# Performance work log

Measured on AMD Instinct MI355X. Metric: run time of the kernel, lower is better.

## Reference

```python
import jax, jax.numpy as jnp
import numpy as np

H = 2048      # hidden_size
NH = 32       # num_heads
NKV = 8       # num_kv_heads
HD = H // NH  # head_dim = 64
G = NH // NKV # num_kv_groups = 4
T = 2048      # seq_len
S = int(T * 0.5)  # num_compressed = 1024
DEPTH = 2
I = 5632      # GatedMLP intermediate size
B = 1
EPS = 1e-6


def _rms_norm(x, w):
    return x * jax.lax.rsqrt(jnp.mean(x * x, axis=-1, keepdims=True) + EPS) * w


def setup_inputs() -> dict:
    key = jax.random.key(0)
    ks = jax.random.split(key, 8)
    s = 0.02
    return {
        "hidden_states": jax.random.normal(ks[0], (B, T, H), jnp.float32),
        "q_w": jax.random.normal(ks[1], (H, H), jnp.float32) * s,
        "k_w": jax.random.normal(ks[2], (NKV * HD, H), jnp.float32) * s,
        "v_w": jax.random.normal(ks[3], (NKV * HD, H), jnp.float32) * s,
        "o_w": jax.random.normal(ks[4], (H, H), jnp.float32) * s,
        "attn_norm_w": jnp.ones((H,), jnp.float32),
        "mlp_norm_w": jnp.ones((H,), jnp.float32),
        "gate_w": jax.random.normal(ks[5], (I, H), jnp.float32) * s,
        "up_w": jax.random.normal(ks[6], (I, H), jnp.float32) * s,
        "down_w": jax.random.normal(ks[7], (H, I), jnp.float32) * s,
    }


def reference(hidden_states, q_w, k_w, v_w, o_w, attn_norm_w, mlp_norm_w,
              gate_w, up_w, down_w):
    b, t, h = hidden_states.shape
    scale = HD ** -0.5
    # suffix init: compressed tokens are the last S tokens
    ct = hidden_states[:, -S:, :]  # [B, S, H]
    for _ in range(DEPTH):
        residual = jnp.concatenate([hidden_states, ct], axis=1)  # [B, T+S, H]
        x = _rms_norm(ct, attn_norm_w)
        q = (x @ q_w.T).reshape(b, S, NH, HD)              # [B,S,NH,HD]
        k = (residual @ k_w.T).reshape(b, t + S, NKV, HD)  # [B,T+S,NKV,HD]
        v = (residual @ v_w.T).reshape(b, t + S, NKV, HD)
        # GQA: repeat_interleave over head dim
        k = jnp.repeat(k, G, axis=2)  # [B,T+S,NH,HD]
        v = jnp.repeat(v, G, axis=2)
        scores = jnp.einsum('bsnk,btnk->bsnt', q, k) * scale  # [B,S,NH,T+S]
        attn = jax.nn.softmax(scores, axis=-1)
        o = jnp.einsum('bsnt,btnk->bsnk', attn, v).reshape(b, S, h)
        ct = o @ o_w.T + ct
        y = _rms_norm(ct, mlp_norm_w)
        mlp = (jax.nn.silu(y @ gate_w.T) * (y @ up_w.T)) @ down_w.T
        ct = mlp + y  # note: residual adds to the *normed* tokens, as in source
    return ct
```

## Files before the change

### kernel.cpp

```cpp
#include <hip/hip_runtime.h>

typedef __attribute__((ext_vector_type(8))) short short8;
typedef __attribute__((ext_vector_type(4))) float f32x4;
typedef __attribute__((ext_vector_type(4))) unsigned short us4;
typedef __attribute__((ext_vector_type(8))) unsigned short us8;

__device__ __forceinline__ unsigned short f2bf(float f) {
  union { float f; unsigned u; } v; v.f = f;
  unsigned r = v.u + 0x7fffu + ((v.u >> 16) & 1u);
  return (unsigned short)(r >> 16);
}
__device__ __forceinline__ float bf2f(unsigned short b) {
  union { unsigned u; float f; } v; v.u = ((unsigned)b) << 16;
  return v.f;
}
__device__ __forceinline__ float fexp2(float x) {
  float r; asm("v_exp_f32 %0, %1" : "=v"(r) : "v"(x)); return r;
}
__device__ __forceinline__ us8 cvt8v(f32x4 a, f32x4 b) {
  us8 o;
  o[0] = f2bf(a[0]); o[1] = f2bf(a[1]); o[2] = f2bf(a[2]); o[3] = f2bf(a[3]);
  o[4] = f2bf(b[0]); o[5] = f2bf(b[1]); o[6] = f2bf(b[2]); o[7] = f2bf(b[3]);
  return o;
}

__device__ __forceinline__ void gload_lds16(const void* g, void* l) {
  __builtin_amdgcn_global_load_lds((const __attribute__((address_space(1))) void*)g,
                                   (__attribute__((address_space(3))) void*)l,
                                   16, 0, 0);
}

#define VMW6() asm volatile("s_waitcnt vmcnt(6)" ::: "memory")
#define VMW0() asm volatile("s_waitcnt vmcnt(0)" ::: "memory")
#define LGKM0() asm volatile("s_waitcnt lgkmcnt(0)" ::: "memory")

template<int R>
__device__ __forceinline__ void stage64(const unsigned short* g, int K, int k0,
                                        unsigned short* lds, int tid) {
  const int lane = tid & 63, w = tid >> 6;
  constexpr int RW = R / 4;
  constexpr int NL = RW / 8;
#pragma unroll
  for (int i = 0; i < NL; i++) {
    const int r0 = w * RW + i * 8;
    const int row = r0 + (lane >> 3);
    const int colb = (((lane & 7) ^ (lane >> 3)) << 4);
    gload_lds16((const char*)(g + (size_t)row * K + k0) + colb, lds + r0 * 64);
  }
}
__device__ __forceinline__ short8 lds_frag(const unsigned short* t, int row, int cb) {
  return *(const short8*)((const char*)t + row * 128 + (cb ^ ((row & 7) << 4)));
}

__global__ __launch_bounds__(256) void gemm_split(
    const unsigned short* __restrict__ A,
    const unsigned short* __restrict__ B,
    int K,
    float* __restrict__ P,
    int ldo)
{
  constexpr int BM = 64, BN = 128, BK = 64;
  __shared__ __align__(16) unsigned short sA[3][BM * BK];
  __shared__ __align__(16) unsigned short sB[3][BN * BK];
  const int tid = threadIdx.x;
  const int lane = tid & 63, w = tid >> 6;
  const int wr = w >> 1, wc = w & 1;
  const int ln = lane & 15, qo = lane >> 4;
  const size_t m0 = (size_t)blockIdx.y * BM, n0 = (size_t)blockIdx.x * BN;
  const int koff = blockIdx.z * (K >> 1);
  const unsigned short* Ab = A + m0 * K;
  const unsigned short* Bb = B + n0 * K;

  const f32x4 z4 = {0.f, 0.f, 0.f, 0.f};
  f32x4 acc[2][4];
#pragma unroll
  for (int i = 0; i < 2; i++)
#pragma unroll
    for (int j = 0; j < 4; j++) acc[i][j] = z4;

  const int nt = K / (2 * BK);
  stage64<BM>(Ab, K, koff, sA[0], tid);
  stage64<BN>(Bb, K, koff, sB[0], tid);
  stage64<BM>(Ab, K, koff + BK, sA[1], tid);
  stage64<BN>(Bb, K, koff + BK, sB[1], tid);

  int cur = 0;
  for (int t = 0; t < nt; ++t) {
    if (t == nt - 1) VMW0(); else VMW6();
    __builtin_amdgcn_s_barrier();
    asm volatile("" ::: "memory");
    if (t + 2 < nt) {
      const int nx = (cur == 0) ? 2 : cur - 1;
      stage64<BM>(Ab, K, koff + (t + 2) * BK, sA[nx], tid);
      stage64<BN>(Bb, K, koff + (t + 2) * BK, sB[nx], tid);
    }
    const unsigned short* cA = sA[cur];
    const unsigned short* cB = sB[cur];
#pragma unroll
    for (int ks = 0; ks < 2; ks++) {
      short8 af[2], bfv[4];
#pragma unroll
      for (int mi = 0; mi < 2; mi++)
        af[mi] = lds_frag(cA, wr * 32 + mi * 16 + ln, ks * 64 + qo * 16);
#pragma unroll
      for (int ni = 0; ni < 4; ni++)
        bfv[ni] = lds_frag(cB, wc * 64 + ni * 16 + ln, ks * 64 + qo * 16);
      __builtin_amdgcn_s_setprio(1);
#pragma unroll
      for (int mi = 0; mi < 2; mi++)
#pragma unroll
        for (int ni = 0; ni < 4; ni++)
          acc[mi][ni] = __builtin_amdgcn_mfma_f32_16x16x32_bf16(af[mi], bfv[ni], acc[mi][ni], 0, 0, 0);
      __builtin_amdgcn_s_setprio(0);
    }
    cur = (cur == 2) ? 0 : cur + 1;
  }

  float* Pz = P + (size_t)blockIdx.z * 1024 * (size_t)ldo;
#pragma unroll
  for (int mi = 0; mi < 2; mi++) {
#pragma unroll
    for (int ni = 0; ni < 4; ni++) {
      const size_t row4 = m0 + wr * 32 + mi * 16 + qo * 4;
      const size_t col  = n0 + wc * 64 + ni * 16 + ln;
#pragma unroll
      for (int r = 0; r < 4; r++)
        Pz[(row4 + r) * (size_t)ldo + col] = acc[mi][ni][r];
    }
  }
}

__global__ __launch_bounds__(256) void gemm_gu(
    const unsigned short* __restrict__ A,
    const unsigned short* __restrict__ B,
    unsigned short* __restrict__ outb)
{
  __shared__ __align__(16) unsigned short sA[2][128 * 64];
  __shared__ __align__(16) unsigned short sB[2][128 * 64];
  const int tid = threadIdx.x;
  const int lane = tid & 63, w = tid >> 6;
  const int wr = w >> 1, wc = w & 1;
  const int ln = lane & 15, qo = lane >> 4;
  const int bid = blockIdx.x;
  const int swz = (bid & 7) * 88 + (bid >> 3);
  const size_t m0 = (size_t)(swz & 7) * 128;
  const size_t n0 = (size_t)(swz >> 3) * 128;
  const unsigned short* Ab = A + m0 * 2048;
  const unsigned short* Bb = B + n0 * 2048;

  const f32x4 z4 = {0.f, 0.f, 0.f, 0.f};
  f32x4 acc[4][4];
#pragma unroll
  for (int i = 0; i < 4; i++)
#pragma unroll
    for (int j = 0; j < 4; j++) acc[i][j] = z4;

  stage64<128>(Ab, 2048, 0, sA[0], tid);
  stage64<128>(Bb, 2048, 0, sB[0], tid);

  for (int t = 0; t < 32; ++t) {
    const int cur = t & 1;
    VMW0();
    __builtin_amdgcn_s_barrier();
    asm volatile("" ::: "memory");
    if (t + 1 < 32) {
      stage64<128>(Ab, 2048, (t + 1) * 64, sA[cur ^ 1], tid);
      stage64<128>(Bb, 2048, (t + 1) * 64, sB[cur ^ 1], tid);
    }
    const unsigned short* cA = sA[cur];
    const unsigned short* cB = sB[cur];
#pragma unroll
    for (int ks = 0; ks < 2; ks++) {
      short8 af[4], bfv[4];
#pragma unroll
      for (int mi = 0; mi < 4; mi++)
        af[mi] = lds_frag(cA, wr * 64 + mi * 16 + ln, ks * 64 + qo * 16);
#pragma unroll
      for (int ni = 0; ni < 4; ni++)
        bfv[ni] = lds_frag(cB, wc * 64 + ni * 16 + ln, ks * 64 + qo * 16);
      __builtin_amdgcn_s_setprio(1);
#pragma unroll
      for (int mi = 0; mi < 4; mi++)
#pragma unroll
        for (int ni = 0; ni < 4; ni++)
          acc[mi][ni] = __builtin_amdgcn_mfma_f32_16x16x32_bf16(af[mi], bfv[ni], acc[mi][ni], 0, 0, 0);
      __builtin_amdgcn_s_setprio(0);
    }
  }

#pragma unroll
  for (int mi = 0; mi < 4; mi++) {
#pragma unroll
    for (int j = 0; j < 2; j++) {
      const size_t row4 = m0 + wr * 64 + mi * 16 + qo * 4;
      const size_t cg = (n0 >> 1) + wc * 32 + j * 16 + ln;
#pragma unroll
      for (int r = 0; r < 4; r++) {
        float g = acc[mi][2 * j][r], u = acc[mi][2 * j + 1][r];
        outb[(row4 + r) * 5632 + cg] = f2bf(g / (1.f + __expf(-g)) * u);
      }
    }
  }
}

template<int SPLIT>
__global__ __launch_bounds__(256) void gemm_dual(
    const unsigned short* __restrict__ A,
    const unsigned short* __restrict__ B0,
    const unsigned short* __restrict__ B1,
    int K,
    unsigned short* __restrict__ out0,
    unsigned short* __restrict__ out1,
    float* __restrict__ P,
    int ld0, int ld1)
{
  constexpr int BM = 64, BN = 64, BK = 64;
  __shared__ __align__(16) unsigned short sA[3][BM * BK];
  __shared__ __align__(16) unsigned short sB0[3][BN * BK];
  __shared__ __align__(16) unsigned short sB1[3][BN * BK];
  const int tid = threadIdx.x;
  const int lane = tid & 63, w = tid >> 6;
  const int wr = w >> 1, wc = w & 1;
  const int ln = lane & 15, qo = lane >> 4;
  const size_t m0 = (size_t)blockIdx.y * BM, n0 = (size_t)blockIdx.x * BN;
  const int koff = SPLIT ? blockIdx.z * (K >> 1) : 0;
  const unsigned short* Ab = A + m0 * K;
  const unsigned short* B0b = B0 + n0 * K;
  const unsigned short* B1b = B1 + n0 * K;

  const f32x4 z4 = {0.f, 0.f, 0.f, 0.f};
  f32x4 acc0[2][2], acc1[2][2];
#pragma unroll
  for (int i = 0; i < 2; i++)
#pragma unroll
    for (int j = 0; j < 2; j++) { acc0[i][j] = z4; acc1[i][j] = z4; }

  const int nt = SPLIT ? K / (2 * BK) : K / BK;
  stage64<BM>(Ab, K, koff, sA[0], tid);
  stage64<BN>(B0b, K, koff, sB0[0], tid);
  stage64<BN>(B1b, K, koff, sB1[0], tid);
  stage64<BM>(Ab, K, koff + BK, sA[1], tid);
  stage64<BN>(B0b, K, koff + BK, sB0[1], tid);
  stage64<BN>(B1b, K, koff + BK, sB1[1], tid);

  int cur = 0;
  for (int t = 0; t < nt; ++t) {
    if (t == nt - 1) VMW0(); else VMW6();
    __builtin_amdgcn_s_barrier();
    asm volatile("" ::: "memory");
    if (t + 2 < nt) {
      const int nx = (cur == 0) ? 2 : cur - 1;
      stage64<BM>(Ab, K, koff + (t + 2) * BK, sA[nx], tid);
      stage64<BN>(B0b, K, koff + (t + 2) * BK, sB0[nx], tid);
      stage64<BN>(B1b, K, koff + (t + 2) * BK, sB1[nx], tid);
    }
    const unsigned short* cA = sA[cur];
    const unsigned short* cB0 = sB0[cur];
    const unsigned short* cB1 = sB1[cur];
#pragma unroll
    for (int ks = 0; ks < 2; ks++) {
      short8 af[2], b0f[2], b1f[2];
#pragma unroll
      for (int mi = 0; mi < 2; mi++)
        af[mi] = lds_frag(cA, wr * 32 + mi * 16 + ln, ks * 64 + qo * 16);
#pragma unroll
      for (int ni = 0; ni < 2; ni++) {
        b0f[ni] = lds_frag(cB0, wc * 32 + ni * 16 + ln, ks * 64 + qo * 16);
        b1f[ni] = lds_frag(cB1, wc * 32 + ni * 16 + ln, ks * 64 + qo * 16);
      }
      __builtin_amdgcn_s_setprio(1);
#pragma unroll
      for (int mi = 0; mi < 2; mi++)
#pragma unroll
        for (int ni = 0; ni < 2; ni++) {
          acc0[mi][ni] = __builtin_amdgcn_mfma_f32_16x16x32_bf16(af[mi], b0f[ni], acc0[mi][ni], 0, 0, 0);
          acc1[mi][ni] = __builtin_amdgcn_mfma_f32_16x16x32_bf16(af[mi], b1f[ni], acc1[mi][ni], 0, 0, 0);
        }
      __builtin_amdgcn_s_setprio(0);
    }
    cur = (cur == 2) ? 0 : cur + 1;
  }

#pragma unroll
  for (int mi = 0; mi < 2; mi++) {
#pragma unroll
    for (int ni = 0; ni < 2; ni++) {
      const size_t row4 = m0 + wr * 32 + mi * 16 + qo * 4;
      const size_t col  = n0 + wc * 32 + ni * 16 + ln;
      if (SPLIT) {
        float* Pz = P + (size_t)blockIdx.z * 1048576;
#pragma unroll
        for (int r = 0; r < 4; r++) {
          Pz[(row4 + r) * 1024 + col] = acc0[mi][ni][r];
          Pz[(row4 + r) * 1024 + 512 + col] = acc1[mi][ni][r];
        }
      } else {
#pragma unroll
        for (int r = 0; r < 4; r++)
          out0[(row4 + r) * (size_t)ld0 + col] = f2bf(acc0[mi][ni][r]);
        us4 pk;
        pk[0] = f2bf(acc1[mi][ni][0]); pk[1] = f2bf(acc1[mi][ni][1]);
        pk[2] = f2bf(acc1[mi][ni][2]); pk[3] = f2bf(acc1[mi][ni][3]);
        *(us4*)&out1[col * (size_t)ld1 + row4] = pk;
      }
    }
  }
}

__global__ __launch_bounds__(256) void combine_kv(
    const float* __restrict__ P,
    unsigned short* __restrict__ kB,
    unsigned short* __restrict__ vt)
{
  const int j = blockIdx.x * 256 + threadIdx.x;
  {
    const int row = j >> 9, col = j & 511;
    float v = P[row * 1024 + col] + P[1048576 + row * 1024 + col];
    kB[row * 512 + col] = f2bf(v);
  }
  {
    const int hd = j >> 10, key = j & 1023;
    float v0 = P[key * 1024 + 512 + hd] + P[1048576 + key * 1024 + 512 + hd];
    vt[(size_t)hd * 3072 + key] = f2bf(v0);
  }
}

__global__ __launch_bounds__(256) void attn_k(
    const float* __restrict__ Pq,
    const unsigned short* __restrict__ Kb,
    const unsigned short* __restrict__ Vt,
    unsigned short* __restrict__ Op,
    float* __restrict__ Ml)
{
  __shared__ __align__(16) unsigned short sK[2][64 * 64];
  __shared__ __align__(16) unsigned short sV[2][64 * 64];
  __shared__ __align__(16) unsigned short sP[64 * 64];
  const int tid = threadIdx.x;
  const int lane = tid & 63, w = tid >> 6;
  const int ln = lane & 15, qo = lane >> 4;
  const int head = blockIdx.y, kvh = head >> 2;
  const int half = blockIdx.z;
  const int qw = blockIdx.x * 64 + w * 16;
  const int key0 = half * 1536;

  const float QS = 0.18033688011112042f;
  const float* qr = Pq + (size_t)(qw + ln) * 2048 + head * 64;
  short8 qf[2];
#pragma unroll
  for (int kc = 0; kc < 2; kc++) {
    const float* q0 = qr + kc * 32 + qo * 8;
    f32x4 a0 = *(const f32x4*)(q0);
    f32x4 a1 = *(const f32x4*)(q0 + 4);
    f32x4 b0 = *(const f32x4*)(q0 + 2097152);
    f32x4 b1 = *(const f32x4*)(q0 + 2097152 + 4);
    short8 t;
    t[0] = (short)f2bf((a0[0] + b0[0]) * QS); t[1] = (short)f2bf((a0[1] + b0[1]) * QS);
    t[2] = (short)f2bf((a0[2] + b0[2]) * QS); t[3] = (short)f2bf((a0[3] + b0[3]) * QS);
    t[4] = (short)f2bf((a1[0] + b1[0]) * QS); t[5] = (short)f2bf((a1[1] + b1[1]) * QS);
    t[6] = (short)f2bf((a1[2] + b1[2]) * QS); t[7] = (short)f2bf((a1[3] + b1[3]) * QS);
    qf[kc] = t;
  }

  const f32x4 z4 = {0.f, 0.f, 0.f, 0.f};
  f32x4 oacc[4] = {z4, z4, z4, z4};
  float mrun = -1e30f, lrun = 0.f;

  const unsigned short* Kg = Kb + kvh * 64;
  const unsigned short* Vg = Vt + (size_t)(kvh * 64) * 3072;

  stage64<64>(Kg + (size_t)key0 * 512, 512, 0, sK[0], tid);
  stage64<64>(Vg, 3072, key0, sV[0], tid);

  for (int t = 0; t < 24; ++t) {
    const int cur = t & 1;
    VMW0();
    __builtin_amdgcn_s_barrier();
    asm volatile("" ::: "memory");
    if (t + 1 < 24) {
      stage64<64>(Kg + (size_t)(key0 + (t + 1) * 64) * 512, 512, 0, sK[cur ^ 1], tid);
      stage64<64>(Vg, 3072, key0 + (t + 1) * 64, sV[cur ^ 1], tid);
    }

    f32x4 sacc[4] = {z4, z4, z4, z4};
#pragma unroll
    for (int kc = 0; kc < 2; kc++) {
      short8 kf[4];
#pragma unroll
      for (int mi = 0; mi < 4; mi++)
        kf[mi] = lds_frag(sK[cur], mi * 16 + ln, kc * 64 + qo * 16);
      __builtin_amdgcn_s_setprio(1);
#pragma unroll
      for (int mi = 0; mi < 4; mi++)
        sacc[mi] = __builtin_amdgcn_mfma_f32_16x16x32_bf16(kf[mi], qf[kc], sacc[mi], 0, 0, 0);
      __builtin_amdgcn_s_setprio(0);
    }

    float tm = -1e30f;
#pragma unroll
    for (int mi = 0; mi < 4; mi++) {
      float a0 = fmaxf(sacc[mi][0], sacc[mi][1]);
      float a1 = fmaxf(sacc[mi][2], sacc[mi][3]);
      tm = fmaxf(tm, fmaxf(a0, a1));
    }
    tm = fmaxf(tm, __shfl_xor(tm, 16));
    tm = fmaxf(tm, __shfl_xor(tm, 32));

    if (!__all(tm <= mrun + 11.f)) {
      const float mn = fmaxf(mrun, tm);
      const float al = fexp2(mrun - mn);
      lrun *= al;
      mrun = mn;
#pragma unroll
      for (int r = 0; r < 4; r++) {
        float ar = __shfl(al, qo * 4 + r);
#pragma unroll
        for (int ni = 0; ni < 4; ni++) oacc[ni][r] *= ar;
      }
    }

    float ts = 0.f;
#pragma unroll
    for (int mi = 0; mi < 4; mi++) {
      us4 pk;
#pragma unroll
      for (int r = 0; r < 4; r++) {
        float pv = fexp2(sacc[mi][r] - mrun);
        ts += pv;
        pk[r] = f2bf(pv);
      }
      const int row = w * 16 + ln;
      const int g16 = (2 * mi + (qo >> 1)) ^ (ln & 7);
      *(us4*)((char*)sP + row * 128 + (g16 << 4) + ((qo & 1) << 3)) = pk;
    }
    ts += __shfl_xor(ts, 16);
    ts += __shfl_xor(ts, 32);
    lrun += ts;

#pragma unroll
    for (int ks = 0; ks < 2; ks++) {
      short8 pf = lds_frag(sP, w * 16 + ln, ks * 64 + qo * 16);
      short8 vf[4];
#pragma unroll
      for (int ni = 0; ni < 4; ni++)
        vf[ni] = lds_frag(sV[cur], ni * 16 + ln, ks * 64 + qo * 16);
      __builtin_amdgcn_s_setprio(1);
#pragma unroll
      for (int ni = 0; ni < 4; ni++)
        oacc[ni] = __builtin_amdgcn_mfma_f32_16x16x32_bf16(pf, vf[ni], oacc[ni], 0, 0, 0);
      __builtin_amdgcn_s_setprio(0);
    }
    LGKM0();
  }

  if (qo == 0)
    *(float2*)&Ml[((size_t)(half * 32 + head) * 1024 + qw + ln) * 2] =
        make_float2(mrun, lrun);
#pragma unroll
  for (int r = 0; r < 4; r++)
#pragma unroll
    for (int ni = 0; ni < 4; ni++)
      Op[(size_t)half * 2097152 + (size_t)(qw + qo * 4 + r) * 2048 + head * 64 + ni * 16 + ln] =
          f2bf(oacc[ni][r]);
}

__global__ __launch_bounds__(256) void attn_combine(
    const unsigned short* __restrict__ Op,
    const float* __restrict__ Ml,
    unsigned short* __restrict__ O)
{
  const int f = blockIdx.x * 256 + threadIdx.x;
  const int q = f >> 9;
  const int c = (f & 511) * 4;
  const int head = c >> 6;
  const float2 ml0 = *(const float2*)&Ml[((size_t)head * 1024 + q) * 2];
  const float2 ml1 = *(const float2*)&Ml[((size_t)(32 + head) * 1024 + q) * 2];
  const float m = fmaxf(ml0.x, ml1.x);
  const float w0 = fexp2(ml0.x - m), w1 = fexp2(ml1.x - m);
  const float inv = 1.f / (w0 * ml0.y + w1 * ml1.y);
  const us4 o0 = *(const us4*)&Op[(size_t)q * 2048 + c];
  const us4 o1 = *(const us4*)&Op[2097152 + (size_t)q * 2048 + c];
  us4 o;
#pragma unroll
  for (int j = 0; j < 4; j++)
    o[j] = f2bf((w0 * bf2f(o0[j]) + w1 * bf2f(o1[j])) * inv);
  *(us4*)&O[(size_t)q * 2048 + c] = o;
}

__global__ __launch_bounds__(256) void rmsnorm_k(const float* __restrict__ in,
                                                 const float* __restrict__ w,
                                                 unsigned short* __restrict__ out) {
  const int row = blockIdx.x;
  const int tid = threadIdx.x;
  const float* x = in + (size_t)row * 2048;
  float4 a = ((const float4*)x)[tid * 2];
  float4 b = ((const float4*)x)[tid * 2 + 1];
  float ss = a.x * a.x + a.y * a.y + a.z * a.z + a.w * a.w +
             b.x * b.x + b.y * b.y + b.z * b.z + b.w * b.w;
#pragma unroll
  for (int d = 1; d < 64; d <<= 1) ss += __shfl_xor(ss, d);
  __shared__ float red[4];
  if ((tid & 63) == 0) red[tid >> 6] = ss;
  __syncthreads();
  float sc = rsqrtf((red[0] + red[1] + red[2] + red[3]) * (1.f / 2048.f) + 1e-6f);
  float4 wa = ((const float4*)w)[tid * 2];
  float4 wb = ((const float4*)w)[tid * 2 + 1];
  us4 o1, o2;
  o1[0] = f2bf(a.x * sc * wa.x); o1[1] = f2bf(a.y * sc * wa.y);
  o1[2] = f2bf(a.z * sc * wa.z); o1[3] = f2bf(a.w * sc * wa.w);
  o2[0] = f2bf(b.x * sc * wb.x); o2[1] = f2bf(b.y * sc * wb.y);
  o2[2] = f2bf(b.z * sc * wb.z); o2[3] = f2bf(b.w * sc * wb.w);
  us4* op = (us4*)&out[(size_t)row * 2048 + tid * 8];
  op[0] = o1; op[1] = o2;
}

__global__ __launch_bounds__(256) void rmsnorm_add_k(
    float* __restrict__ ctf, const float* __restrict__ P,
    const float* __restrict__ w, unsigned short* __restrict__ out) {
  const int row = blockIdx.x;
  const int tid = threadIdx.x;
  const size_t base = (size_t)row * 2048 + tid * 8;
  float t[8];
  float4 c0 = *(const float4*)&ctf[base], c1 = *(const float4*)&ctf[base + 4];
  float4 p0 = *(const float4*)&P[base], p1 = *(const float4*)&P[base + 4];
  float4 q0 = *(const float4*)&P[base + 2097152], q1 = *(const float4*)&P[base + 2097152 + 4];
  t[0] = c0.x + p0.x + q0.x; t[1] = c0.y + p0.y + q0.y;
  t[2] = c0.z + p0.z + q0.z; t[3] = c0.w + p0.w + q0.w;
  t[4] = c1.x + p1.x + q1.x; t[5] = c1.y + p1.y + q1.y;
  t[6] = c1.z + p1.z + q1.z; t[7] = c1.w + p1.w + q1.w;
  *(float4*)&ctf[base] = make_float4(t[0], t[1], t[2], t[3]);
  *(float4*)&ctf[base + 4] = make_float4(t[4], t[5], t[6], t[7]);
  float ss = 0.f;
#pragma unroll
  for (int i = 0; i < 8; i++) ss += t[i] * t[i];
#pragma unroll
  for (int d = 1; d < 64; d <<= 1) ss += __shfl_xor(ss, d);
  __shared__ float red[4];
  if ((tid & 63) == 0) red[tid >> 6] = ss;
  __syncthreads();
  float sc = rsqrtf((red[0] + red[1] + red[2] + red[3]) * (1.f / 2048.f) + 1e-6f);
  us4 o1, o2;
#pragma unroll
  for (int i = 0; i < 4; i++) o1[i] = f2bf(t[i] * sc * w[tid * 8 + i]);
#pragma unroll
  for (int i = 0; i < 4; i++) o2[i] = f2bf(t[4 + i] * sc * w[tid * 8 + 4 + i]);
  us4* op = (us4*)&out[base];
  op[0] = o1; op[1] = o2;
}

__global__ __launch_bounds__(256) void rmsnorm_add2_k(
    const float* __restrict__ P, unsigned short* __restrict__ yb,
    float* __restrict__ ctf, unsigned short* __restrict__ ctb,
    const float* __restrict__ w) {
  const int row = blockIdx.x;
  const int tid = threadIdx.x;
  const size_t base = (size_t)row * 2048 + tid * 8;
  float t[8];
  float4 p0 = *(const float4*)&P[base], p1 = *(const float4*)&P[base + 4];
  float4 q0 = *(const float4*)&P[base + 2097152], q1 = *(const float4*)&P[base + 2097152 + 4];
  us4 y0 = *(const us4*)&yb[base], y1 = *(const us4*)&yb[base + 4];
  t[0] = p0.x + q0.x + bf2f(y0[0]); t[1] = p0.y + q0.y + bf2f(y0[1]);
  t[2] = p0.z + q0.z + bf2f(y0[2]); t[3] = p0.w + q0.w + bf2f(y0[3]);
  t[4] = p1.x + q1.x + bf2f(y1[0]); t[5] = p1.y + q1.y + bf2f(y1[1]);
  t[6] = p1.z + q1.z + bf2f(y1[2]); t[7] = p1.w + q1.w + bf2f(y1[3]);
  *(float4*)&ctf[base] = make_float4(t[0], t[1], t[2], t[3]);
  *(float4*)&ctf[base + 4] = make_float4(t[4], t[5], t[6], t[7]);
  us4 cb0, cb1;
#pragma unroll
  for (int i = 0; i < 4; i++) { cb0[i] = f2bf(t[i]); cb1[i] = f2bf(t[4 + i]); }
  *(us4*)&ctb[base] = cb0; *(us4*)&ctb[base + 4] = cb1;
  float ss = 0.f;
#pragma unroll
  for (int i = 0; i < 8; i++) ss += t[i] * t[i];
#pragma unroll
  for (int d = 1; d < 64; d <<= 1) ss += __shfl_xor(ss, d);
  __shared__ float red[4];
  if ((tid & 63) == 0) red[tid >> 6] = ss;
  __syncthreads();
  float sc = rsqrtf((red[0] + red[1] + red[2] + red[3]) * (1.f / 2048.f) + 1e-6f);
  us4 o1, o2;
#pragma unroll
  for (int i = 0; i < 4; i++) o1[i] = f2bf(t[i] * sc * w[tid * 8 + i]);
#pragma unroll
  for (int i = 0; i < 4; i++) o2[i] = f2bf(t[4 + i] * sc * w[tid * 8 + 4 + i]);
  us4* op = (us4*)&yb[base];
  op[0] = o1; op[1] = o2;
}

__global__ __launch_bounds__(256) void combine2_k(
    const float* __restrict__ P, const unsigned short* __restrict__ yb,
    float* __restrict__ out) {
  const int j = blockIdx.x * 256 + threadIdx.x;
  float4 p0 = ((const float4*)P)[j];
  float4 p1 = ((const float4*)P)[j + 524288];
  us4 y = ((const us4*)yb)[j];
  float4 o;
  o.x = p0.x + p1.x + bf2f(y[0]); o.y = p0.y + p1.y + bf2f(y[1]);
  o.z = p0.z + p1.z + bf2f(y[2]); o.w = p0.w + p1.w + bf2f(y[3]);
  ((float4*)out)[j] = o;
}

__global__ __launch_bounds__(256) void cvt_all(
    const float* __restrict__ hid, const float* __restrict__ qw,
    const float* __restrict__ kw, const float* __restrict__ vw,
    const float* __restrict__ ow, const float* __restrict__ gw,
    const float* __restrict__ uw, const float* __restrict__ dw,
    unsigned short* __restrict__ hb, unsigned short* __restrict__ qwB,
    unsigned short* __restrict__ kwB, unsigned short* __restrict__ vwB,
    unsigned short* __restrict__ owB, unsigned short* __restrict__ guB,
    unsigned short* __restrict__ dwB,
    float* __restrict__ ctf, unsigned short* __restrict__ ctb)
{
  const int gid = blockIdx.x * 256 + threadIdx.x;
  const int gs = gridDim.x * 256;
  for (int i = gid; i < 524288; i += gs) {
    f32x4 a = __builtin_nontemporal_load(&((const f32x4*)hid)[2 * i]);
    f32x4 b = __builtin_nontemporal_load(&((const f32x4*)hid)[2 * i + 1]);
    us8 o = cvt8v(a, b);
    ((us8*)hb)[i] = o;
    if (i >= 262144) {
      ((f32x4*)ctf)[2 * (i - 262144)] = a;
      ((f32x4*)ctf)[2 * (i - 262144) + 1] = b;
      ((us8*)ctb)[i - 262144] = o;
    }
  }
  for (int i = gid; i < 524288; i += gs) {
    f32x4 a = __builtin_nontemporal_load(&((const f32x4*)qw)[2 * i]);
    f32x4 b = __builtin_nontemporal_load(&((const f32x4*)qw)[2 * i + 1]);
    ((us8*)qwB)[i] = cvt8v(a, b);
  }
  for (int i = gid; i < 131072; i += gs) {
    f32x4 a = __builtin_nontemporal_load(&((const f32x4*)kw)[2 * i]);
    f32x4 b = __builtin_nontemporal_load(&((const f32x4*)kw)[2 * i + 1]);
    ((us8*)kwB)[i] = cvt8v(a, b);
  }
  for (int i = gid; i < 131072; i += gs) {
    f32x4 a = __builtin_nontemporal_load(&((const f32x4*)vw)[2 * i]);
    f32x4 b = __builtin_nontemporal_load(&((const f32x4*)vw)[2 * i + 1]);
    ((us8*)vwB)[i] = cvt8v(a, b);
  }
  for (int i = gid; i < 524288; i += gs) {
    f32x4 a = __builtin_nontemporal_load(&((const f32x4*)ow)[2 * i]);
    f32x4 b = __builtin_nontemporal_load(&((const f32x4*)ow)[2 * i + 1]);
    ((us8*)owB)[i] = cvt8v(a, b);
  }
  for (int i = gid; i < 1441792; i += gs) {
    f32x4 a = __builtin_nontemporal_load(&((const f32x4*)gw)[2 * i]);
    f32x4 b = __builtin_nontemporal_load(&((const f32x4*)gw)[2 * i + 1]);
    const int row = i >> 8, c8 = i & 255;
    const int drow = ((row >> 4) << 5) + (row & 15);
    ((us8*)guB)[(drow << 8) + c8] = cvt8v(a, b);
  }
  for (int i = gid; i < 1441792; i += gs) {
    f32x4 a = __builtin_nontemporal_load(&((const f32x4*)uw)[2 * i]);
    f32x4 b = __builtin_nontemporal_load(&((const f32x4*)uw)[2 * i + 1]);
    const int row = i >> 8, c8 = i & 255;
    const int drow = ((row >> 4) << 5) + (row & 15) + 16;
    ((us8*)guB)[(drow << 8) + c8] = cvt8v(a, b);
  }
  for (int i = gid; i < 1441792; i += gs) {
    f32x4 a = __builtin_nontemporal_load(&((const f32x4*)dw)[2 * i]);
    f32x4 b = __builtin_nontemporal_load(&((const f32x4*)dw)[2 * i + 1]);
    ((us8*)dwB)[i] = cvt8v(a, b);
  }
}

extern "C" void kernel_launch(void* const* d_in, const int* in_sizes, int n_in,
                              void* d_out, int out_size, void* d_ws, size_t ws_size,
                              hipStream_t stream) {
  (void)in_sizes; (void)n_in; (void)out_size; (void)ws_size;
  const float* hidden = (const float*)d_in[0];
  const float* q_w  = (const float*)d_in[1];
  const float* k_w  = (const float*)d_in[2];
  const float* v_w  = (const float*)d_in[3];
  const float* o_w  = (const float*)d_in[4];
  const float* a_nw = (const float*)d_in[5];
  const float* m_nw = (const float*)d_in[6];
  const float* g_w  = (const float*)d_in[7];
  const float* u_w  = (const float*)d_in[8];
  const float* dn_w = (const float*)d_in[9];
  float* out = (float*)d_out;

  char* p = (char*)d_ws;
  size_t off = 0;
  auto take = [&](size_t bytes) -> char* {
    char* r = p + off;
    off += (bytes + 255) & ~(size_t)255;
    return r;
  };
  float* ctf          = (float*)take((size_t)1024 * 2048 * 4);
  unsigned short* ctb = (unsigned short*)take((size_t)1024 * 2048 * 2);
  unsigned short* xb  = (unsigned short*)take((size_t)1024 * 2048 * 2);
  unsigned short* hb  = (unsigned short*)take((size_t)2048 * 2048 * 2);
  unsigned short* qwB = (unsigned short*)take((size_t)2048 * 2048 * 2);
  unsigned short* kwB = (unsigned short*)take((size_t)512 * 2048 * 2);
  unsigned short* vwB = (unsigned short*)take((size_t)512 * 2048 * 2);
  unsigned short* owB = (unsigned short*)take((size_t)2048 * 2048 * 2);
  unsigned short* guB = (unsigned short*)take((size_t)11264 * 2048 * 2);
  unsigned short* dwB = (unsigned short*)take((size_t)2048 * 5632 * 2);
  unsigned short* kB  = (unsigned short*)take((size_t)3072 * 512 * 2);
  unsigned short* vtB = (unsigned short*)take((size_t)512 * 3072 * 2);
  unsigned short* oB  = (unsigned short*)take((size_t)1024 * 2048 * 2);
  unsigned short* gtB = (unsigned short*)take((size_t)1024 * 5632 * 2);
  float* Pd           = (float*)take((size_t)2 * 1024 * 2048 * 4);

  unsigned short* Op = xb;
  float* Ml = (float*)((char*)xb + (size_t)2 * 1024 * 2048 * 2);
  float* PKV = (float*)hb;

  dim3 blk(256);
  cvt_all<<<dim3(4096), blk, 0, stream>>>(hidden, q_w, k_w, v_w, o_w, g_w, u_w, dn_w,
                                          hb, qwB, kwB, vwB, owB, guB, dwB, ctf, ctb);

  gemm_dual<0><<<dim3(8, 32), blk, 0, stream>>>(hb, kwB, vwB, 2048, kB, vtB, nullptr, 512, 3072);

  for (int it = 0; it < 2; it++) {
    if (it == 0)
      rmsnorm_k<<<dim3(1024), blk, 0, stream>>>(ctf, a_nw, xb);
    else
      rmsnorm_add2_k<<<dim3(1024), blk, 0, stream>>>(Pd, xb, ctf, ctb, a_nw);
    gemm_split<<<dim3(16, 16, 2), blk, 0, stream>>>(xb, qwB, 2048, Pd, 2048);
    gemm_dual<1><<<dim3(8, 16, 2), blk, 0, stream>>>(ctb, kwB, vwB, 2048,
                                                     nullptr, nullptr, PKV, 0, 0);
    combine_kv<<<dim3(2048), blk, 0, stream>>>(PKV, kB + (size_t)2048 * 512, vtB + 2048);
    attn_k<<<dim3(16, 32, 2), blk, 0, stream>>>(Pd, kB, vtB, Op, Ml);
    attn_combine<<<dim3(2048), blk, 0, stream>>>(Op, Ml, oB);
    gemm_split<<<dim3(16, 16, 2), blk, 0, stream>>>(oB, owB, 2048, Pd, 2048);
    rmsnorm_add_k<<<dim3(1024), blk, 0, stream>>>(ctf, Pd, m_nw, xb);
    gemm_gu<<<dim3(704), blk, 0, stream>>>(xb, guB, gtB);
    gemm_split<<<dim3(16, 16, 2), blk, 0, stream>>>(gtB, dwB, 5632, Pd, 2048);
  }
  combine2_k<<<dim3(2048), blk, 0, stream>>>(Pd, xb, out);
}
```

Baseline: 577.1 us.

## Triple-buffer gate/up GEMM and attention K/V staging with prefetch depth two

The gate/up GEMM moves from double-buffered BK=64 tiles to triple-buffered BK=32 tiles, using a new packed LDS layout that puts two 32-wide rows in one 128-byte line with an XOR swizzle. Prefetch now runs two iterations ahead and waits with a partial vmcnt instead of draining to zero. The attention kernel's K/V staging is likewise changed to three buffers with a two-ahead prefetch and partial waits. The aim is to hide global-load latency behind MFMA work, at the cost of more barriers per unit of compute in the GEMM and more LDS use in attention, which may reduce occupancy.

```diff
diff --git a/kernel.cpp b/kernel.cpp
--- a/kernel.cpp
+++ b/kernel.cpp
@@ -31,6 +31,7 @@
 }
 
 #define VMW6() asm volatile("s_waitcnt vmcnt(6)" ::: "memory")
+#define VMW4() asm volatile("s_waitcnt vmcnt(4)" ::: "memory")
 #define VMW0() asm volatile("s_waitcnt vmcnt(0)" ::: "memory")
 #define LGKM0() asm volatile("s_waitcnt lgkmcnt(0)" ::: "memory")
 
@@ -50,6 +51,29 @@
 }
 __device__ __forceinline__ short8 lds_frag(const unsigned short* t, int row, int cb) {
   return *(const short8*)((const char*)t + row * 128 + (cb ^ ((row & 7) << 4)));
+}
+
+template<int GR>
+__device__ __forceinline__ void stage32p(const unsigned short* g, int K, int k0,
+                                         unsigned short* lds, int tid) {
+  const int lane = tid & 63, w = tid >> 6;
+  constexpr int LR = GR / 2;
+  constexpr int RW = LR / 4;
+  constexpr int NL = RW / 8;
+#pragma unroll
+  for (int i = 0; i < NL; i++) {
+    const int R0 = w * RW + i * 8;
+    const int R = R0 + (lane >> 3);
+    const int gg = (lane & 7) ^ (R & 7);
+    const int grow = 2 * R + (gg >> 2);
+    const int gcol = (gg & 3) * 8;
+    gload_lds16(g + (size_t)grow * K + k0 + gcol, lds + R0 * 64);
+  }
+}
+__device__ __forceinline__ short8 frag32p(const unsigned short* t, int grow, int qo) {
+  const int R = grow >> 1;
+  const int g16 = (((grow & 1) << 2) + qo) ^ (R & 7);
+  return *(const short8*)((const char*)t + R * 128 + (g16 << 4));
 }
 
 __global__ __launch_bounds__(256) void gemm_split(
@@ -135,8 +159,8 @@
     const unsigned short* __restrict__ B,
     unsigned short* __restrict__ outb)
 {
-  __shared__ __align__(16) unsigned short sA[2][128 * 64];
-  __shared__ __align__(16) unsigned short sB[2][128 * 64];
+  __shared__ __align__(16) unsigned short sA[3][64 * 64];
+  __shared__ __align__(16) unsigned short sB[3][64 * 64];
   const int tid = threadIdx.x;
   const int lane = tid & 63, w = tid >> 6;
   const int wr = w >> 1, wc = w & 1;
@@ -155,37 +179,39 @@
 #pragma unroll
     for (int j = 0; j < 4; j++) acc[i][j] = z4;
 
-  stage64<128>(Ab, 2048, 0, sA[0], tid);
-  stage64<128>(Bb, 2048, 0, sB[0], tid);
-
-  for (int t = 0; t < 32; ++t) {
-    const int cur = t & 1;
-    VMW0();
+  const int nt = 64;
+  stage32p<128>(Ab, 2048, 0, sA[0], tid);
+  stage32p<128>(Bb, 2048, 0, sB[0], tid);
+  stage32p<128>(Ab, 2048, 32, sA[1], tid);
+  stage32p<128>(Bb, 2048, 32, sB[1], tid);
+
+  int cur = 0;
+  for (int t = 0; t < nt; ++t) {
+    if (t == nt - 1) VMW0(); else VMW4();
     __builtin_amdgcn_s_barrier();
     asm volatile("" ::: "memory");
-    if (t + 1 < 32) {
-      stage64<128>(Ab, 2048, (t + 1) * 64, sA[cur ^ 1], tid);
-      stage64<128>(Bb, 2048, (t + 1) * 64, sB[cur ^ 1], tid);
+    if (t + 2 < nt) {
+      const int nx = (cur == 0) ? 2 : cur - 1;
+      stage32p<128>(Ab, 2048, (t + 2) * 32, sA[nx], tid);
+      stage32p<128>(Bb, 2048, (t + 2) * 32, sB[nx], tid);
     }
     const unsigned short* cA = sA[cur];
     const unsigned short* cB = sB[cur];
-#pragma unroll
-    for (int ks = 0; ks < 2; ks++) {
-      short8 af[4], bfv[4];
-#pragma unroll
-      for (int mi = 0; mi < 4; mi++)
-        af[mi] = lds_frag(cA, wr * 64 + mi * 16 + ln, ks * 64 + qo * 16);
+    short8 af[4], bfv[4];
+#pragma unroll
+    for (int mi = 0; mi < 4; mi++)
+      af[mi] = frag32p(cA, wr * 64 + mi * 16 + ln, qo);
+#pragma unroll
+    for (int ni = 0; ni < 4; ni++)
+      bfv[ni] = frag32p(cB, wc * 64 + ni * 16 + ln, qo);
+    __builtin_amdgcn_s_setprio(1);
+#pragma unroll
+    for (int mi = 0; mi < 4; mi++)
 #pragma unroll
       for (int ni = 0; ni < 4; ni++)
-        bfv[ni] = lds_frag(cB, wc * 64 + ni * 16 + ln, ks * 64 + qo * 16);
-      __builtin_amdgcn_s_setprio(1);
-#pragma unroll
-      for (int mi = 0; mi < 4; mi++)
-#pragma unroll
-        for (int ni = 0; ni < 4; ni++)
-          acc[mi][ni] = __builtin_amdgcn_mfma_f32_16x16x32_bf16(af[mi], bfv[ni], acc[mi][ni], 0, 0, 0);
-      __builtin_amdgcn_s_setprio(0);
-    }
+        acc[mi][ni] = __builtin_amdgcn_mfma_f32_16x16x32_bf16(af[mi], bfv[ni], acc[mi][ni], 0, 0, 0);
+    __builtin_amdgcn_s_setprio(0);
+    cur = (cur == 2) ? 0 : cur + 1;
   }
 
 #pragma unroll
@@ -332,8 +358,8 @@
     unsigned short* __restrict__ Op,
     float* __restrict__ Ml)
 {
-  __shared__ __align__(16) unsigned short sK[2][64 * 64];
-  __shared__ __align__(16) unsigned short sV[2][64 * 64];
+  __shared__ __align__(16) unsigned short sK[3][64 * 64];
+  __shared__ __align__(16) unsigned short sV[3][64 * 64];
   __shared__ __align__(16) unsigned short sP[64 * 64];
   const int tid = threadIdx.x;
   const int lane = tid & 63, w = tid >> 6;
@@ -370,15 +396,18 @@
 
   stage64<64>(Kg + (size_t)key0 * 512, 512, 0, sK[0], tid);
   stage64<64>(Vg, 3072, key0, sV[0], tid);
-
+  stage64<64>(Kg + (size_t)(key0 + 64) * 512, 512, 0, sK[1], tid);
+  stage64<64>(Vg, 3072, key0 + 64, sV[1], tid);
+
+  int cur = 0;
   for (int t = 0; t < 24; ++t) {
-    const int cur = t & 1;
-    VMW0();
+    if (t == 23) VMW0(); else VMW4();
     __builtin_amdgcn_s_barrier();
     asm volatile("" ::: "memory");
-    if (t + 1 < 24) {
-      stage64<64>(Kg + (size_t)(key0 + (t + 1) * 64) * 512, 512, 0, sK[cur ^ 1], tid);
-      stage64<64>(Vg, 3072, key0 + (t + 1) * 64, sV[cur ^ 1], tid);
+    if (t + 2 < 24) {
+      const int nx = (cur == 0) ? 2 : cur - 1;
+      stage64<64>(Kg + (size_t)(key0 + (t + 2) * 64) * 512, 512, 0, sK[nx], tid);
+      stage64<64>(Vg, 3072, key0 + (t + 2) * 64, sV[nx], tid);
     }
 
     f32x4 sacc[4] = {z4, z4, z4, z4};
@@ -450,6 +479,7 @@
       __builtin_amdgcn_s_setprio(0);
     }
     LGKM0();
+    cur = (cur == 2) ? 0 : cur + 1;
   }
 
   if (qo == 0)
```

Measured after the change: 570.9 us. Within noise of the previous version (-1.1%).
